# Performance work log

Hardware: AMD Instinct MI355X
Metric: run time of the kernel (lower is better)

Reference implementation:

```python
import jax, jax.numpy as jnp
import numpy as np

NUM_HEADS = 8
RADIUS = 127          # local_attention_radius -> block_length = 128
RMAX = 64             # rel_pos_max_distance -> R = 2*RMAX+1 = 129


def setup_inputs() -> dict:
    key = jax.random.key(0)
    ks = jax.random.split(key, 9)
    B, S, D = 2, 4096, 512
    hd = D // NUM_HEADS
    R = 2 * RMAX + 1
    w = lambda k, shape: 0.02 * jax.random.normal(k, shape, jnp.float32)
    return {
        "Q": jax.random.normal(ks[0], (B, S, D), jnp.float32),
        "K": jax.random.normal(ks[1], (B, S, D), jnp.float32),
        "V": jax.random.normal(ks[2], (B, S, D), jnp.float32),
        "segment_ids": jnp.zeros((B, S), jnp.int32),
        "Wq": w(ks[3], (D, D)),
        "Wk": w(ks[4], (D, D)),
        "Wv": w(ks[5], (D, D)),
        "Wo": w(ks[6], (D, D)),
        "rel_emb": w(ks[7], (NUM_HEADS, R, hd)),
    }


def reference(Q, K, V, segment_ids, Wq, Wk, Wv, Wo, rel_emb):
    B, S, D = Q.shape
    h = NUM_HEADS
    hd = D // h
    bl = RADIUS + 1                      # block length
    nb = -(-S // bl)                     # num query blocks
    pad = nb * bl - S                    # 0 for S divisible by bl
    norm = float(hd) ** 0.5

    def proj(X, W):  # B x S x D -> B x h x S x hd
        return (X @ W).reshape(B, S, h, hd).transpose(0, 2, 1, 3)

    q = proj(Q, Wq)
    k = proj(K, Wk)
    v = proj(V, Wv)

    # query blocks: B x h x nb x bl x hd
    qb = jnp.pad(q, ((0, 0), (0, 0), (0, pad), (0, 0))).reshape(B, h, nb, bl, hd)
    # sliding key/value blocks: pad bl on each side, gather 3*bl window per block
    kp = jnp.pad(k, ((0, 0), (0, 0), (bl, bl + pad), (0, 0)))
    vp = jnp.pad(v, ((0, 0), (0, 0), (bl, bl + pad), (0, 0)))
    slid = jnp.arange(3 * bl)[None, :] + bl * jnp.arange(nb)[:, None]  # nb x 3bl
    kb = kp[:, :, slid, :]  # B x h x nb x 3bl x hd
    vb = vp[:, :, slid, :]

    energy = jnp.einsum("bhnqd,bhnkd->bhnqk", qb, kb)  # B x h x nb x bl x 3bl

    # relative position bias: Q @ rel_embeds^T then gather by rel pos ids
    qrel = jnp.einsum("bhnqd,hrd->bhnqr", qb, rel_emb)  # B x h x nb x bl x R
    i = jnp.arange(bl)
    j = jnp.arange(3 * bl)
    dpos = j[None, :] - bl - i[:, None]                 # bl x 3bl, key - query offset
    ids = jnp.clip(dpos, -RMAX, RMAX) + RMAX            # bl x 3bl in [0, 2*RMAX]
    rel_shift = qrel[:, :, :, i[:, None], ids]          # B x h x nb x bl x 3bl

    energy = (energy + rel_shift) / norm

    # mask: out-of-sequence keys and keys beyond local radius
    kg = bl * jnp.arange(nb)[:, None, None] + (j - bl)[None, None, :]
    invalid = (kg < 0) | (kg >= S) | (jnp.abs(dpos)[None] > RADIUS)    # nb x bl x 3bl
    energy = jnp.where(invalid[None, None], -jnp.inf, energy)

    attn = jax.nn.softmax(energy, axis=-1)
    outb = jnp.einsum("bhnqk,bhnkd->bhnqd", attn, vb)   # B x h x nb x bl x hd
    out = outb.reshape(B, h, nb * bl, hd)[:, :, :S, :]  # B x h x S x hd
    # torch code interleaves features as (head_dim, head): permute(0,2,3,1).flatten(2,3)
    out = out.transpose(0, 2, 3, 1).reshape(B, S, hd * h)
    return out @ Wo
```

## Files before the change

### kernel.cpp

```cpp
#include <hip/hip_runtime.h>
#include <hip/hip_bf16.h>

typedef unsigned short u16;
typedef __bf16 bf16_t;
typedef bf16_t bf16x8 __attribute__((ext_vector_type(8)));
typedef float f32x4 __attribute__((ext_vector_type(4)));
typedef u16 u16x4 __attribute__((ext_vector_type(4)));
typedef u16 u16x8 __attribute__((ext_vector_type(8)));

#define S_LEN 4096
#define NH 8
#define HD 64
#define DM 512
#define NB 32

__device__ __forceinline__ u16 f2bf(float f) {
  unsigned int u = __builtin_bit_cast(unsigned int, f);
  u = (u + 0x7fff + ((u >> 16) & 1)) >> 16;
  return (u16)u;
}
__device__ __forceinline__ float bf2f(u16 h) {
  unsigned int u = ((unsigned int)h) << 16;
  return __builtin_bit_cast(float, u);
}

#define GLDS16(gaddr, laddr)                                                  \
  __builtin_amdgcn_global_load_lds(                                           \
      (const __attribute__((address_space(1))) unsigned int*)(gaddr),         \
      (__attribute__((address_space(3))) unsigned int*)(laddr), 16, 0, 0)

__global__ __launch_bounds__(256) void conv_big(
    const float* __restrict__ Q, const float* __restrict__ K,
    const float* __restrict__ V, u16* __restrict__ Qb, u16* __restrict__ Kb,
    u16* __restrict__ Vb) {
  const int z = blockIdx.y;
  const float* src = z == 0 ? Q : (z == 1 ? K : V);
  u16* dst = z == 0 ? Qb : (z == 1 ? Kb : Vb);
  const size_t idx = ((size_t)blockIdx.x * 256 + threadIdx.x) * 4;
  const float4 v = *(const float4*)(src + idx);
  u16x4 o;
  o[0] = f2bf(v.x); o[1] = f2bf(v.y); o[2] = f2bf(v.z); o[3] = f2bf(v.w);
  *(u16x4*)(dst + idx) = o;
}

__global__ __launch_bounds__(256) void conv_w(
    const float* __restrict__ Wq, const float* __restrict__ Wk,
    const float* __restrict__ Wv, const float* __restrict__ Wo,
    u16* __restrict__ WqT, u16* __restrict__ WkT, u16* __restrict__ WvT,
    u16* __restrict__ WoT) {
  const int z = blockIdx.y;
  const float* src = z == 0 ? Wq : (z == 1 ? Wk : (z == 2 ? Wv : Wo));
  u16* dst = z == 0 ? WqT : (z == 1 ? WkT : (z == 2 ? WvT : WoT));
  const float scl = (z == 0) ? 0.125f : 1.f;
  const int idx4 = blockIdx.x * 256 + threadIdx.x;
  const int nrow = idx4 >> 7;
  const int kbase = (idx4 & 127) * 4;
  u16x4 o;
#pragma unroll
  for (int j = 0; j < 4; ++j) {
    const int k = kbase + j;
    const int srow = (z == 3) ? ((k & 63) * 8 + (k >> 6)) : k;
    o[j] = f2bf(src[srow * DM + nrow] * scl);
  }
  *(u16x4*)(dst + nrow * DM + kbase) = o;
}

__global__ __launch_bounds__(128) void conv_rel(const float* __restrict__ rel,
                                                u16* __restrict__ relb) {
  const int e = (blockIdx.x * 128 + threadIdx.x) * 4;
  const int h = e / (129 * 64);
  const int rem = e - h * (129 * 64);
  const float4 v = *(const float4*)(rel + e);
  u16x4 o;
  o[0] = f2bf(v.x); o[1] = f2bf(v.y); o[2] = f2bf(v.z); o[3] = f2bf(v.w);
  *(u16x4*)(relb + (size_t)h * (144 * 64) + rem) = o;
}

template <int MODE>
__global__ __launch_bounds__(256, 2) void gemm_bf16(
    const u16* __restrict__ A0, const u16* __restrict__ A1,
    const u16* __restrict__ A2, const u16* __restrict__ B0,
    const u16* __restrict__ B1, const u16* __restrict__ B2,
    u16* __restrict__ C0, u16* __restrict__ C1, u16* __restrict__ C2,
    float* __restrict__ Cf) {
  __shared__ u16 As[128 * 32];
  __shared__ u16 Bs[128 * 32];

  const int z = blockIdx.z;
  const u16* A = (MODE == 1) ? (z == 0 ? A0 : (z == 1 ? A1 : A2)) : A0;
  const u16* Bt = (MODE == 1) ? (z == 0 ? B0 : (z == 1 ? B1 : B2)) : B0;
  u16* Cb = (MODE == 1) ? (z == 0 ? C0 : (z == 1 ? C1 : C2)) : (u16*)0;

  const int tid = threadIdx.x;
  const int lane = tid & 63;
  const int w = tid >> 6;
  const int bm = blockIdx.x * 128;
  const int bn = blockIdx.y * 128;

  const int srow = lane >> 2;
  const int scol = (lane & 3) * 8;

  f32x4 acc[4][4];
#pragma unroll
  for (int m = 0; m < 4; ++m)
#pragma unroll
    for (int nf = 0; nf < 4; ++nf) acc[m][nf] = f32x4{0.f, 0.f, 0.f, 0.f};

  const int wr = w >> 1, wc = w & 1;
  const int lrow = lane & 15;
  const int lk = (lane >> 4) * 8;

  for (int k0 = 0; k0 < DM; k0 += 32) {
#pragma unroll
    for (int t = 0; t < 2; ++t) {
      const int c = t * 4 + w;
      const int ar = c * 16 + srow;
      long gidx;
      if (MODE == 2) {
        const int r = bm + ar;
        const int b = r >> 12, s = r & 4095;
        const int k = k0 + scol;
        gidx = ((long)((b * 8 + (k >> 6)) * 4096 + s)) * 64 + (k & 63);
      } else {
        gidx = (long)(bm + ar) * DM + k0 + scol;
      }
      GLDS16(A + gidx, &As[c * 512]);
      const long bidx = (long)(bn + ar) * DM + k0 + scol;
      GLDS16(Bt + bidx, &Bs[c * 512]);
    }
    __syncthreads();

    bf16x8 af[4], bfr[4];
#pragma unroll
    for (int m = 0; m < 4; ++m)
      af[m] = *(const bf16x8*)&As[(wr * 64 + m * 16 + lrow) * 32 + lk];
#pragma unroll
    for (int nf = 0; nf < 4; ++nf)
      bfr[nf] = *(const bf16x8*)&Bs[(wc * 64 + nf * 16 + lrow) * 32 + lk];
#pragma unroll
    for (int m = 0; m < 4; ++m)
#pragma unroll
      for (int nf = 0; nf < 4; ++nf)
        acc[m][nf] = __builtin_amdgcn_mfma_f32_16x16x32_bf16(
            af[m], bfr[nf], acc[m][nf], 0, 0, 0);
    __syncthreads();
  }

  const int lr4 = (lane >> 4) * 4;
  const int lc = lane & 15;
#pragma unroll
  for (int m = 0; m < 4; ++m) {
#pragma unroll
    for (int nf = 0; nf < 4; ++nf) {
#pragma unroll
      for (int j = 0; j < 4; ++j) {
        const int r = bm + wr * 64 + m * 16 + lr4 + j;
        const int cg = bn + wc * 64 + nf * 16 + lc;
        const float val = acc[m][nf][j];
        if (MODE == 1) {
          const int b = r >> 12, s = r & 4095;
          Cb[((long)((b * 8 + (cg >> 6)) * 4096 + s)) * 64 + (cg & 63)] =
              f2bf(val);
        } else {
          Cf[(long)r * DM + cg] = val;
        }
      }
    }
  }
}

__global__ __launch_bounds__(256, 2) void attn_mfma(
    const u16* __restrict__ qg, const u16* __restrict__ kgl,
    const u16* __restrict__ vgl, const u16* __restrict__ relb,
    u16* __restrict__ pre) {
  const int n = blockIdx.x, hh = blockIdx.y, b = blockIdx.z;
  const int tid = threadIdx.x;
  const int lane = tid & 63, w = tid >> 6;
  const int g = lane >> 4, lc = lane & 15;

  __shared__ u16 Ks[64 * 72];
  __shared__ u16 Vt[64 * 72];
  __shared__ u16 Pl[4][32 * 72];
  __shared__ u16 qrelL[128 * 132];

  const size_t bh = (size_t)(b * NH + hh);

  const u16* qbase = qg + (bh * S_LEN + (size_t)n * 128 + w * 32) * HD;
  bf16x8 qf[2][2];
#pragma unroll
  for (int qt = 0; qt < 2; ++qt)
#pragma unroll
    for (int dc = 0; dc < 2; ++dc)
      qf[qt][dc] =
          *(const bf16x8*)(qbase + (lc + 16 * qt) * HD + g * 8 + 32 * dc);

  const u16* rh = relb + (size_t)hh * (144 * 64);
#pragma unroll
  for (int rt = 0; rt < 9; ++rt) {
    f32x4 acc[2] = {{0.f, 0.f, 0.f, 0.f}, {0.f, 0.f, 0.f, 0.f}};
#pragma unroll
    for (int dc = 0; dc < 2; ++dc) {
      const bf16x8 rf =
          *(const bf16x8*)(rh + (lc + 16 * rt) * 64 + g * 8 + 32 * dc);
#pragma unroll
      for (int qt = 0; qt < 2; ++qt)
        acc[qt] = __builtin_amdgcn_mfma_f32_16x16x32_bf16(qf[qt][dc], rf,
                                                          acc[qt], 0, 0, 0);
    }
#pragma unroll
    for (int qt = 0; qt < 2; ++qt)
#pragma unroll
      for (int jj = 0; jj < 4; ++jj)
        qrelL[(w * 32 + qt * 16 + g * 4 + jj) * 132 + lc + 16 * rt] =
            f2bf(acc[qt][jj]);
  }

  float m_r[2][4], l_r[2][4];
  f32x4 Oa[2][4];
#pragma unroll
  for (int qt = 0; qt < 2; ++qt)
#pragma unroll
    for (int jj = 0; jj < 4; ++jj) {
      m_r[qt][jj] = -1e30f;
      l_r[qt][jj] = 0.f;
    }
#pragma unroll
  for (int qt = 0; qt < 2; ++qt)
#pragma unroll
    for (int dt = 0; dt < 4; ++dt) Oa[qt][dt] = f32x4{0.f, 0.f, 0.f, 0.f};

  const u16* kbase = kgl + bh * S_LEN * HD;
  const u16* vbase = vgl + bh * S_LEN * HD;
  const int sk = tid & 63;
  const int sd = (tid >> 6) * 16;

  const int t0 = (n == 0) ? 2 : 0;
  const int t1 = (n == NB - 1) ? 4 : 6;

  for (int t = t0; t < t1; ++t) {
    {
      const int kglob = n * 128 - 128 + t * 64 + sk;
      const int kc = min(max(kglob, 0), S_LEN - 1);
      const u16* krow = kbase + (size_t)kc * HD + sd;
      const u16* vrow = vbase + (size_t)kc * HD + sd;
      const u16x8 ka = *(const u16x8*)krow;
      const u16x8 kb2 = *(const u16x8*)(krow + 8);
      const u16x8 va = *(const u16x8*)vrow;
      const u16x8 vb2 = *(const u16x8*)(vrow + 8);
      *(u16x8*)&Ks[sk * 72 + sd] = ka;
      *(u16x8*)&Ks[sk * 72 + sd + 8] = kb2;
#pragma unroll
      for (int e = 0; e < 8; ++e) {
        Vt[(sd + e) * 72 + sk] = va[e];
        Vt[(sd + 8 + e) * 72 + sk] = vb2[e];
      }
    }
    __syncthreads();

    f32x4 E[2][4];
#pragma unroll
    for (int qt = 0; qt < 2; ++qt)
#pragma unroll
      for (int kt = 0; kt < 4; ++kt) E[qt][kt] = f32x4{0.f, 0.f, 0.f, 0.f};
#pragma unroll
    for (int kt = 0; kt < 4; ++kt)
#pragma unroll
      for (int dc = 0; dc < 2; ++dc) {
        const bf16x8 kf =
            *(const bf16x8*)&Ks[(lc + 16 * kt) * 72 + g * 8 + 32 * dc];
#pragma unroll
        for (int qt = 0; qt < 2; ++qt)
          E[qt][kt] = __builtin_amdgcn_mfma_f32_16x16x32_bf16(qf[qt][dc], kf,
                                                              E[qt][kt], 0, 0, 0);
      }

#pragma unroll
    for (int qt = 0; qt < 2; ++qt)
#pragma unroll
      for (int jj = 0; jj < 4; ++jj) {
        const int q = w * 32 + qt * 16 + g * 4 + jj;
#pragma unroll
        for (int kt = 0; kt < 4; ++kt) {
          const int j = t * 64 + kt * 16 + lc;
          const int dpos = j - 128 - q;
          const int kglob = n * 128 - 128 + j;
          const int idc = min(max(dpos, -64), 64) + 64;
          const float bias = bf2f(qrelL[q * 132 + idc]);
          const float e = E[qt][kt][jj] + bias;
          const bool bad = (dpos > 127) || (dpos < -127) ||
                           ((unsigned)kglob >= (unsigned)S_LEN);
          E[qt][kt][jj] = bad ? -1e30f : e;
        }
      }

#pragma unroll
    for (int qt = 0; qt < 2; ++qt)
#pragma unroll
      for (int jj = 0; jj < 4; ++jj) {
        float mx = fmaxf(fmaxf(E[qt][0][jj], E[qt][1][jj]),
                         fmaxf(E[qt][2][jj], E[qt][3][jj]));
        mx = fmaxf(mx, __shfl_xor(mx, 1));
        mx = fmaxf(mx, __shfl_xor(mx, 2));
        mx = fmaxf(mx, __shfl_xor(mx, 4));
        mx = fmaxf(mx, __shfl_xor(mx, 8));
        const float nm = fmaxf(m_r[qt][jj], mx);
        const float sc = __expf(m_r[qt][jj] - nm);
        m_r[qt][jj] = nm;
        l_r[qt][jj] *= sc;
#pragma unroll
        for (int dt = 0; dt < 4; ++dt) Oa[qt][dt][jj] *= sc;
        float ps = 0.f;
#pragma unroll
        for (int kt = 0; kt < 4; ++kt) {
          const float p = __expf(E[qt][kt][jj] - nm);
          ps += p;
          Pl[w][(qt * 16 + g * 4 + jj) * 72 + lc + 16 * kt] = f2bf(p);
        }
        ps += __shfl_xor(ps, 1);
        ps += __shfl_xor(ps, 2);
        ps += __shfl_xor(ps, 4);
        ps += __shfl_xor(ps, 8);
        l_r[qt][jj] += ps;
      }
    __syncthreads();

#pragma unroll
    for (int c = 0; c < 2; ++c) {
      bf16x8 pf[2];
#pragma unroll
      for (int qt = 0; qt < 2; ++qt)
        pf[qt] = *(const bf16x8*)&Pl[w][(lc + 16 * qt) * 72 + g * 8 + 32 * c];
#pragma unroll
      for (int dt = 0; dt < 4; ++dt) {
        const bf16x8 vf =
            *(const bf16x8*)&Vt[(lc + 16 * dt) * 72 + g * 8 + 32 * c];
#pragma unroll
        for (int qt = 0; qt < 2; ++qt)
          Oa[qt][dt] = __builtin_amdgcn_mfma_f32_16x16x32_bf16(pf[qt], vf,
                                                               Oa[qt][dt], 0, 0, 0);
      }
    }
    __syncthreads();
  }

  u16* prow = pre + (bh * S_LEN + (size_t)n * 128 + w * 32) * HD;
#pragma unroll
  for (int qt = 0; qt < 2; ++qt)
#pragma unroll
    for (int jj = 0; jj < 4; ++jj) {
      const float inv = 1.f / l_r[qt][jj];
      const int row = qt * 16 + g * 4 + jj;
#pragma unroll
      for (int dt = 0; dt < 4; ++dt)
        prow[row * HD + lc + 16 * dt] = f2bf(Oa[qt][dt][jj] * inv);
    }
}

extern "C" void kernel_launch(void* const* d_in, const int* in_sizes, int n_in,
                              void* d_out, int out_size, void* d_ws,
                              size_t ws_size, hipStream_t stream) {
  const float* Q = (const float*)d_in[0];
  const float* K = (const float*)d_in[1];
  const float* V = (const float*)d_in[2];
  const float* Wq = (const float*)d_in[4];
  const float* Wk = (const float*)d_in[5];
  const float* Wv = (const float*)d_in[6];
  const float* Wo = (const float*)d_in[7];
  const float* rel = (const float*)d_in[8];
  float* out = (float*)d_out;

  const size_t NE = 4194304;
  u16* ws16 = (u16*)d_ws;
  u16* Qb = ws16;
  u16* Kb = Qb + NE;
  u16* Vb = Kb + NE;
  u16* qb = Vb + NE;
  u16* kb = qb + NE;
  u16* vb = kb + NE;
  u16* WqT = vb + NE;
  u16* WkT = WqT + 262144;
  u16* WvT = WkT + 262144;
  u16* WoT = WvT + 262144;
  u16* relb = WoT + 262144;
  u16* pre = Qb;

  conv_big<<<dim3(4096, 3), 256, 0, stream>>>(Q, K, V, Qb, Kb, Vb);
  conv_w<<<dim3(256, 4), 256, 0, stream>>>(Wq, Wk, Wv, Wo, WqT, WkT, WvT, WoT);
  conv_rel<<<dim3(129), 128, 0, stream>>>(rel, relb);
  gemm_bf16<1><<<dim3(64, 4, 3), 256, 0, stream>>>(Qb, Kb, Vb, WqT, WkT, WvT,
                                                   qb, kb, vb, nullptr);
  attn_mfma<<<dim3(NB, NH, 2), 256, 0, stream>>>(qb, kb, vb, relb, pre);
  gemm_bf16<2><<<dim3(64, 4, 1), 256, 0, stream>>>(
      pre, nullptr, nullptr, WoT, nullptr, nullptr, nullptr, nullptr, nullptr,
      out);
}
```

Measured before the change: 189.1 us.

## Double-buffer GEMM tiles, vectorize epilogue stores, add lazy softmax rescale

The GEMM kernel now double-buffers its LDS tiles, issuing the next k-slice load while the current one is multiplied. It also swaps the MFMA operands so each lane holds four consecutive columns, which lets the epilogue use 4-wide vector stores. In attention, the key-bounds mask is reduced to a single radius check, and the online-softmax rescale is skipped when the new row max stays within a threshold of the running max. The lazy rescale can let unnormalized exponents grow by up to e^8, which is a numerical risk, and the masking change assumes out-of-range keys are already handled elsewhere (for example by zero padding).

New measurement: 185.0 us. -2.2%, faster.

```diff
diff --git a/kernel.cpp b/kernel.cpp
--- a/kernel.cpp
+++ b/kernel.cpp
@@ -83,8 +83,8 @@
     const u16* __restrict__ B1, const u16* __restrict__ B2,
     u16* __restrict__ C0, u16* __restrict__ C1, u16* __restrict__ C2,
     float* __restrict__ Cf) {
-  __shared__ u16 As[128 * 32];
-  __shared__ u16 Bs[128 * 32];
+  __shared__ u16 As[2][128 * 32];
+  __shared__ u16 Bs[2][128 * 32];
 
   const int z = blockIdx.z;
   const u16* A = (MODE == 1) ? (z == 0 ? A0 : (z == 1 ? A1 : A2)) : A0;
@@ -110,7 +110,7 @@
   const int lrow = lane & 15;
   const int lk = (lane >> 4) * 8;
 
-  for (int k0 = 0; k0 < DM; k0 += 32) {
+  auto stage = [&](int buf, int k0) {
 #pragma unroll
     for (int t = 0; t < 2; ++t) {
       const int c = t * 4 + w;
@@ -124,25 +124,32 @@
       } else {
         gidx = (long)(bm + ar) * DM + k0 + scol;
       }
-      GLDS16(A + gidx, &As[c * 512]);
+      GLDS16(A + gidx, &As[buf][c * 512]);
       const long bidx = (long)(bn + ar) * DM + k0 + scol;
-      GLDS16(Bt + bidx, &Bs[c * 512]);
-    }
-    __syncthreads();
+      GLDS16(Bt + bidx, &Bs[buf][c * 512]);
+    }
+  };
+
+  stage(0, 0);
+  __syncthreads();
+
+  for (int t = 0; t < 16; ++t) {
+    const int cur = t & 1;
+    if (t < 15) stage(cur ^ 1, (t + 1) * 32);
 
     bf16x8 af[4], bfr[4];
 #pragma unroll
     for (int m = 0; m < 4; ++m)
-      af[m] = *(const bf16x8*)&As[(wr * 64 + m * 16 + lrow) * 32 + lk];
+      af[m] = *(const bf16x8*)&As[cur][(wr * 64 + m * 16 + lrow) * 32 + lk];
 #pragma unroll
     for (int nf = 0; nf < 4; ++nf)
-      bfr[nf] = *(const bf16x8*)&Bs[(wc * 64 + nf * 16 + lrow) * 32 + lk];
+      bfr[nf] = *(const bf16x8*)&Bs[cur][(wc * 64 + nf * 16 + lrow) * 32 + lk];
 #pragma unroll
     for (int m = 0; m < 4; ++m)
 #pragma unroll
       for (int nf = 0; nf < 4; ++nf)
         acc[m][nf] = __builtin_amdgcn_mfma_f32_16x16x32_bf16(
-            af[m], bfr[nf], acc[m][nf], 0, 0, 0);
+            bfr[nf], af[m], acc[m][nf], 0, 0, 0);
     __syncthreads();
   }
 
@@ -150,20 +157,22 @@
   const int lc = lane & 15;
 #pragma unroll
   for (int m = 0; m < 4; ++m) {
+    const int r = bm + wr * 64 + m * 16 + lc;
+    const int bi = r >> 12, s = r & 4095;
 #pragma unroll
     for (int nf = 0; nf < 4; ++nf) {
-#pragma unroll
-      for (int j = 0; j < 4; ++j) {
-        const int r = bm + wr * 64 + m * 16 + lr4 + j;
-        const int cg = bn + wc * 64 + nf * 16 + lc;
-        const float val = acc[m][nf][j];
-        if (MODE == 1) {
-          const int b = r >> 12, s = r & 4095;
-          Cb[((long)((b * 8 + (cg >> 6)) * 4096 + s)) * 64 + (cg & 63)] =
-              f2bf(val);
-        } else {
-          Cf[(long)r * DM + cg] = val;
-        }
+      const int cg = bn + wc * 64 + nf * 16 + lr4;
+      if (MODE == 1) {
+        u16x4 o;
+#pragma unroll
+        for (int j = 0; j < 4; ++j) o[j] = f2bf(acc[m][nf][j]);
+        *(u16x4*)&Cb[((long)((bi * 8 + (cg >> 6)) * 4096 + s)) * 64 +
+                     (cg & 63)] = o;
+      } else {
+        float4 o;
+        o.x = acc[m][nf][0]; o.y = acc[m][nf][1];
+        o.z = acc[m][nf][2]; o.w = acc[m][nf][3];
+        *(float4*)&Cf[(long)r * DM + cg] = o;
       }
     }
   }
@@ -270,8 +279,8 @@
             *(const bf16x8*)&Ks[(lc + 16 * kt) * 72 + g * 8 + 32 * dc];
 #pragma unroll
         for (int qt = 0; qt < 2; ++qt)
-          E[qt][kt] = __builtin_amdgcn_mfma_f32_16x16x32_bf16(qf[qt][dc], kf,
-                                                              E[qt][kt], 0, 0, 0);
+          E[qt][kt] = __builtin_amdgcn_mfma_f32_16x16x32_bf16(
+              qf[qt][dc], kf, E[qt][kt], 0, 0, 0);
       }
 
 #pragma unroll
@@ -283,16 +292,16 @@
         for (int kt = 0; kt < 4; ++kt) {
           const int j = t * 64 + kt * 16 + lc;
           const int dpos = j - 128 - q;
-          const int kglob = n * 128 - 128 + j;
           const int idc = min(max(dpos, -64), 64) + 64;
           const float bias = bf2f(qrelL[q * 132 + idc]);
           const float e = E[qt][kt][jj] + bias;
-          const bool bad = (dpos > 127) || (dpos < -127) ||
-                           ((unsigned)kglob >= (unsigned)S_LEN);
+          const bool bad = ((unsigned)(dpos + 127) > 254u);
           E[qt][kt][jj] = bad ? -1e30f : e;
         }
       }
 
+    float mxv[2][4];
+    bool loc = true;
 #pragma unroll
     for (int qt = 0; qt < 2; ++qt)
 #pragma unroll
@@ -303,16 +312,30 @@
         mx = fmaxf(mx, __shfl_xor(mx, 2));
         mx = fmaxf(mx, __shfl_xor(mx, 4));
         mx = fmaxf(mx, __shfl_xor(mx, 8));
-        const float nm = fmaxf(m_r[qt][jj], mx);
-        const float sc = __expf(m_r[qt][jj] - nm);
-        m_r[qt][jj] = nm;
-        l_r[qt][jj] *= sc;
-#pragma unroll
-        for (int dt = 0; dt < 4; ++dt) Oa[qt][dt][jj] *= sc;
+        mxv[qt][jj] = mx;
+        loc = loc && (mx <= m_r[qt][jj] + 8.f);
+      }
+    if (!__all(loc)) {
+#pragma unroll
+      for (int qt = 0; qt < 2; ++qt)
+#pragma unroll
+        for (int jj = 0; jj < 4; ++jj) {
+          const float nm = fmaxf(m_r[qt][jj], mxv[qt][jj]);
+          const float sc = __expf(m_r[qt][jj] - nm);
+          m_r[qt][jj] = nm;
+          l_r[qt][jj] *= sc;
+#pragma unroll
+          for (int dt = 0; dt < 4; ++dt) Oa[qt][dt][jj] *= sc;
+        }
+    }
+#pragma unroll
+    for (int qt = 0; qt < 2; ++qt)
+#pragma unroll
+      for (int jj = 0; jj < 4; ++jj) {
         float ps = 0.f;
 #pragma unroll
         for (int kt = 0; kt < 4; ++kt) {
-          const float p = __expf(E[qt][kt][jj] - nm);
+          const float p = __expf(E[qt][kt][jj] - m_r[qt][jj]);
           ps += p;
           Pl[w][(qt * 16 + g * 4 + jj) * 72 + lc + 16 * kt] = f2bf(p);
         }
@@ -336,8 +359,8 @@
             *(const bf16x8*)&Vt[(lc + 16 * dt) * 72 + g * 8 + 32 * c];
 #pragma unroll
         for (int qt = 0; qt < 2; ++qt)
-          Oa[qt][dt] = __builtin_amdgcn_mfma_f32_16x16x32_bf16(pf[qt], vf,
-                                                               Oa[qt][dt], 0, 0, 0);
+          Oa[qt][dt] = __builtin_amdgcn_mfma_f32_16x16x32_bf16(
+              pf[qt], vf, Oa[qt][dt], 0, 0, 0);
       }
     }
     __syncthreads();
```
